# Performance work log

Measured on AMD Instinct MI355X. Metric: run time of the kernel, lower is better.

The kernel has to match this reference:

```python
import jax, jax.numpy as jnp
import numpy as np

B, T0, T1, WIDTH, N, K, H = 1, 512, 1536, 2048, 16, 4, 128
T = T0 + T1
THETA = 1000000.0
ROT = H // 2          # partial_rotary_factor = 0.5 -> rotary dim 64
EPS = 1e-6
NEG = -2.3819763e38


def _rmsnorm(x, scale):
    var = jnp.mean(jnp.square(x.astype(jnp.float32)), axis=-1, keepdims=True)
    normed = x * jnp.reciprocal(jnp.sqrt(var + EPS))
    return (normed * (1.0 + scale)).astype(x.dtype)


def _rope(x, cos, sin):
    # x: [B,T,n,H]; rotate first ROT dims (rotate-half convention), pass-through rest
    xr, xp = x[..., :ROT], x[..., ROT:]
    x1, x2 = jnp.split(xr, 2, axis=-1)
    rot = jnp.concatenate([x1 * cos - x2 * sin, x2 * cos + x1 * sin], axis=-1)
    return jnp.concatenate([rot, xp], axis=-1)


def _stream(x, tm, qg_w, k_w, v_w, qn, kn):
    x = x * tm[..., None].astype(x.dtype)
    qg = jnp.einsum('btd,ndh->btnh', x, qg_w)     # [B,t,N,2H]
    q, gate = jnp.split(qg, 2, axis=-1)
    q = _rmsnorm(q, qn)
    k = _rmsnorm(jnp.einsum('btd,kdh->btkh', x, k_w), kn)
    v = jnp.einsum('btd,kdh->btkh', x, v_w)
    return q, k, v, gate


def setup_inputs():
    key = jax.random.key(0)
    ks = jax.random.split(key, 10)
    f = jnp.float32
    sd = WIDTH ** -0.5
    so = (N * H) ** -0.5
    inp = {}
    inp['x0'] = jax.random.normal(ks[0], (B, T0, WIDTH), f)
    inp['x1'] = jax.random.normal(ks[1], (B, T1, WIDTH), f)
    inp['positions'] = jnp.broadcast_to(jnp.arange(T, dtype=jnp.int32), (B, T))
    inp['attn_mask'] = jnp.broadcast_to(jnp.tril(jnp.ones((T, T), bool)), (B, T, T))
    inp['qg_w0'] = jax.random.normal(ks[2], (N, WIDTH, 2 * H), f) * sd
    inp['k_w0'] = jax.random.normal(ks[3], (K, WIDTH, H), f) * sd
    inp['v_w0'] = jax.random.normal(ks[4], (K, WIDTH, H), f) * sd
    inp['qn0'] = jnp.zeros((H,), f)
    inp['kn0'] = jnp.zeros((H,), f)
    inp['o_w0'] = jax.random.normal(ks[5], (N, H, WIDTH), f) * so
    inp['qg_w1'] = jax.random.normal(ks[6], (N, WIDTH, 2 * H), f) * sd
    inp['k_w1'] = jax.random.normal(ks[7], (K, WIDTH, H), f) * sd
    inp['v_w1'] = jax.random.normal(ks[8], (K, WIDTH, H), f) * sd
    inp['qn1'] = jnp.zeros((H,), f)
    inp['kn1'] = jnp.zeros((H,), f)
    inp['o_w1'] = jax.random.normal(ks[9], (N, H, WIDTH), f) * so
    return inp


def reference(x0, x1, positions, attn_mask,
              qg_w0, k_w0, v_w0, qn0, kn0, o_w0,
              qg_w1, k_w1, v_w1, qn1, kn1, o_w1):
    token_mask = jnp.any(attn_mask, axis=-1)  # [B,T]
    q0, k0, v0, g0 = _stream(x0, token_mask[:, :T0], qg_w0, k_w0, v_w0, qn0, kn0)
    q1, k1, v1, g1 = _stream(x1, token_mask[:, T0:], qg_w1, k_w1, v_w1, qn1, kn1)
    q = jnp.concatenate([q0, q1], axis=1)      # [B,T,N,H]
    k = jnp.concatenate([k0, k1], axis=1)      # [B,T,K,H]
    v = jnp.concatenate([v0, v1], axis=1)
    gate = jnp.concatenate([g0, g1], axis=1)

    half = ROT // 2
    inv_freq = THETA ** (-jnp.arange(half, dtype=jnp.float32) / half)
    ang = positions.astype(jnp.float32)[:, :, None] * inv_freq   # [B,T,half]
    cos = jnp.cos(ang)[:, :, None, :]
    sin = jnp.sin(ang)[:, :, None, :]
    q = _rope(q, cos, sin)
    k = _rope(k, cos, sin)
    q = q * (H ** -0.5)

    cached_k, cached_v = k, v                  # kv_cache is None (prefill)
    rep = N // K
    k = jnp.repeat(k, rep, axis=2)             # [B,T,N,H]
    v = jnp.repeat(v, rep, axis=2)

    mask = attn_mask[:, None, :, :]            # [B,1,T,S]
    logits = jnp.einsum('btnh,bsnh->bnts', q, k, preferred_element_type=jnp.float32)
    masked = jnp.where(mask, logits, NEG)
    probs = jax.nn.softmax(masked, axis=-1).astype(q.dtype)
    probs = probs * jnp.any(mask, axis=-1, keepdims=True).astype(q.dtype)
    enc = jnp.einsum('bnts,bsnh->btnh', probs, v)
    enc = enc * jax.nn.sigmoid(gate).astype(enc.dtype)
    out0 = jnp.einsum('btnh,nhd->btd', enc[:, :T0], o_w0)
    out1 = jnp.einsum('btnh,nhd->btd', enc[:, T0:], o_w1)
    return (out0, out1, cached_k, cached_v)
```

## Files before the change

kernel.cpp:

```cpp
#include <hip/hip_runtime.h>
#include <hip/hip_bf16.h>
#include <cstdint>
#include <cstddef>

#define T0_ 512
#define TT_ 2048
#define WD_ 2048
#define NH_ 16
#define KH_ 4

typedef __attribute__((ext_vector_type(8))) short short8;
typedef __attribute__((ext_vector_type(4))) short short4v;
typedef __attribute__((ext_vector_type(4))) float f32x4;

#define AS1 __attribute__((address_space(1)))
#define AS3 __attribute__((address_space(3)))

__device__ __forceinline__ ushort f2bf(float x) {
  __hip_bfloat16 h = __float2bfloat16(x);
  ushort u; __builtin_memcpy(&u, &h, 2); return u;
}
__device__ __forceinline__ float bf2f(ushort u) {
  __hip_bfloat16 h; __builtin_memcpy(&h, &u, 2);
  return __bfloat162float(h);
}
__device__ __forceinline__ void g2l16(const ushort* g, AS3 ushort* s) {
  __builtin_amdgcn_global_load_lds((const AS1 uint32_t*)g, (AS3 uint32_t*)s, 16, 0, 0);
}

__global__ __launch_bounds__(256) void convert_x(
    const float* __restrict__ x0, const float* __restrict__ x1, ushort* __restrict__ xb)
{
  const int i = blockIdx.x * 256 + threadIdx.x;
  const int e = i * 4;
  const int row = e >> 11, col = e & 2047;
  const float* src = (row < T0_) ? (x0 + (size_t)row * WD_ + col)
                                 : (x1 + (size_t)(row - T0_) * WD_ + col);
  const float4 v = *(const float4*)src;
  ushort4 o; o.x = f2bf(v.x); o.y = f2bf(v.y); o.z = f2bf(v.z); o.w = f2bf(v.w);
  *(ushort4*)(xb + e) = o;
}

__global__ __launch_bounds__(256) void convtrans(
    const float* __restrict__ in, ushort* __restrict__ out, int R, int C)
{
  __shared__ float tile[32][33];
  const int z = blockIdx.z;
  in  += (size_t)z * R * C;
  out += (size_t)z * R * C;
  const int r0 = blockIdx.x * 32, c0 = blockIdx.y * 32;
  const int tx = threadIdx.x & 31, ty = threadIdx.x >> 5;
#pragma unroll
  for (int i = 0; i < 4; ++i)
    tile[ty + 8 * i][tx] = in[(size_t)(r0 + ty + 8 * i) * C + c0 + tx];
  __syncthreads();
#pragma unroll
  for (int i = 0; i < 4; ++i)
    out[(size_t)(c0 + ty + 8 * i) * R + r0 + tx] = f2bf(tile[tx][ty + 8 * i]);
}

__global__ __launch_bounds__(256) void convtrans2(
    const float* __restrict__ s0, const float* __restrict__ s1,
    ushort* __restrict__ d0, ushort* __restrict__ d1, int R, int C, int half)
{
  __shared__ float tile[32][33];
  int z = blockIdx.z;
  const float* in; ushort* out;
  if (z < half) { in = s0 + (size_t)z * R * C; out = d0 + (size_t)z * R * C; }
  else { z -= half; in = s1 + (size_t)z * R * C; out = d1 + (size_t)z * R * C; }
  const int r0 = blockIdx.x * 32, c0 = blockIdx.y * 32;
  const int tx = threadIdx.x & 31, ty = threadIdx.x >> 5;
#pragma unroll
  for (int i = 0; i < 4; ++i)
    tile[ty + 8 * i][tx] = in[(size_t)(r0 + ty + 8 * i) * C + c0 + tx];
  __syncthreads();
#pragma unroll
  for (int i = 0; i < 4; ++i)
    out[(size_t)(c0 + ty + 8 * i) * R + r0 + tx] = f2bf(tile[tx][ty + 8 * i]);
}

__device__ __forceinline__ void gemm_core(
    const ushort* __restrict__ A, const ushort* __restrict__ Bt,
    int row0, int col0, ushort* As, ushort* Bs, f32x4 (&acc)[4][4])
{
  const int tid = threadIdx.x;
  const int w = tid >> 6, l = tid & 63, lq = l >> 4, lm = l & 15;
  const int wr = (w >> 1) * 64, wc = (w & 1) * 64;
  const int sx = lm & 7;
  const int gsw = (tid & 7) ^ ((tid >> 3) & 7);
  const ushort* Ag = A + (size_t)(row0 + (tid >> 3)) * WD_ + gsw * 8;
  const ushort* Bg = Bt + (size_t)(col0 + (tid >> 3)) * WD_ + gsw * 8;
  AS3 ushort* AsW = (AS3 ushort*)As + w * 512;
  AS3 ushort* BsW = (AS3 ushort*)Bs + w * 512;

  auto stage = [&](int buf, int k0) {
#pragma unroll
    for (int c = 0; c < 4; ++c) {
      g2l16(Ag + (size_t)(c * 32) * WD_ + k0, AsW + buf * 8192 + c * 2048);
      g2l16(Bg + (size_t)(c * 32) * WD_ + k0, BsW + buf * 8192 + c * 2048);
    }
  };

  stage(0, 0);
  __syncthreads();
  int buf = 0;
  for (int k0 = 0; k0 < WD_; k0 += 64) {
    if (k0 + 64 < WD_) stage(buf ^ 1, k0 + 64);
    const ushort* Ab = As + buf * 8192;
    const ushort* Bb = Bs + buf * 8192;
#pragma unroll
    for (int kk = 0; kk < 2; ++kk) {
      short8 af[4], bfr[4];
#pragma unroll
      for (int mi = 0; mi < 4; ++mi)
        af[mi] = *(const short8*)&Ab[(wr + mi * 16 + lm) * 64 + (((kk * 4 + lq) ^ sx) << 3)];
#pragma unroll
      for (int ni = 0; ni < 4; ++ni)
        bfr[ni] = *(const short8*)&Bb[(wc + ni * 16 + lm) * 64 + (((kk * 4 + lq) ^ sx) << 3)];
#pragma unroll
      for (int mi = 0; mi < 4; ++mi)
#pragma unroll
        for (int ni = 0; ni < 4; ++ni)
          acc[mi][ni] = __builtin_amdgcn_mfma_f32_16x16x32_bf16(af[mi], bfr[ni], acc[mi][ni], 0, 0, 0);
    }
    __syncthreads();
    buf ^= 1;
  }
}

__global__ __launch_bounds__(256) void gemm_proj(
    const ushort* __restrict__ A,
    const ushort* __restrict__ qg0t, const ushort* __restrict__ qg1t,
    const ushort* __restrict__ k0t,  const ushort* __restrict__ k1t,
    const ushort* __restrict__ v0t,  const ushort* __restrict__ v1t,
    ushort* __restrict__ Cqg, float* __restrict__ kc, float* __restrict__ vc)
{
  __shared__ ushort As[16384], Bs[16384];
  const int bx = blockIdx.x;
  const int row0 = blockIdx.y * 128;
  const bool s1 = (row0 >= T0_);
  const ushort* Bt; int col0;
  float* Cf = nullptr; ushort* Cb = nullptr; int ldc;
  if (bx < 32) {
    Bt = s1 ? qg1t : qg0t; col0 = bx * 128; Cb = Cqg; ldc = 4096;
  } else if (bx < 36) {
    Bt = s1 ? k1t : k0t; col0 = (bx - 32) * 128; Cf = kc; ldc = 512;
  } else {
    Bt = s1 ? v1t : v0t; col0 = (bx - 36) * 128; Cf = vc; ldc = 512;
  }
  f32x4 acc[4][4];
#pragma unroll
  for (int mi = 0; mi < 4; ++mi)
#pragma unroll
    for (int ni = 0; ni < 4; ++ni) acc[mi][ni] = (f32x4){0.f, 0.f, 0.f, 0.f};
  gemm_core(A, Bt, row0, col0, As, Bs, acc);
  const int w = threadIdx.x >> 6, l = threadIdx.x & 63, lq = l >> 4, lm = l & 15;
  const int wr = (w >> 1) * 64, wc = (w & 1) * 64;
#pragma unroll
  for (int mi = 0; mi < 4; ++mi)
#pragma unroll
    for (int ni = 0; ni < 4; ++ni)
#pragma unroll
      for (int r = 0; r < 4; ++r) {
        const size_t rr = (size_t)row0 + wr + mi * 16 + lq * 4 + r;
        const size_t cc = (size_t)col0 + wc + ni * 16 + lm;
        if (Cb) Cb[rr * ldc + cc] = f2bf(acc[mi][ni][r]);
        else    Cf[rr * ldc + cc] = acc[mi][ni][r];
      }
}

__global__ __launch_bounds__(256) void gemm_out(
    const ushort* __restrict__ A, const ushort* __restrict__ W0t,
    const ushort* __restrict__ W1t, float* __restrict__ C)
{
  __shared__ ushort As[16384], Bs[16384];
  const int row0 = blockIdx.y * 128, col0 = blockIdx.x * 128;
  const ushort* Bt = (row0 < T0_) ? W0t : W1t;
  f32x4 acc[4][4];
#pragma unroll
  for (int mi = 0; mi < 4; ++mi)
#pragma unroll
    for (int ni = 0; ni < 4; ++ni) acc[mi][ni] = (f32x4){0.f, 0.f, 0.f, 0.f};
  gemm_core(A, Bt, row0, col0, As, Bs, acc);
  const int w = threadIdx.x >> 6, l = threadIdx.x & 63, lq = l >> 4, lm = l & 15;
  const int wr = (w >> 1) * 64, wc = (w & 1) * 64;
#pragma unroll
  for (int mi = 0; mi < 4; ++mi)
#pragma unroll
    for (int ni = 0; ni < 4; ++ni)
#pragma unroll
      for (int r = 0; r < 4; ++r) {
        const size_t rr = (size_t)row0 + wr + mi * 16 + lq * 4 + r;
        const size_t cc = (size_t)col0 + wc + ni * 16 + lm;
        C[rr * 2048 + cc] = acc[mi][ni][r];
      }
}

__global__ __launch_bounds__(256) void postproc(
    ushort* __restrict__ qgb, float* __restrict__ kc, ushort* __restrict__ Kb,
    const int* __restrict__ positions,
    const float* __restrict__ qn0, const float* __restrict__ kn0,
    const float* __restrict__ qn1, const float* __restrict__ kn1)
{
  const int t = blockIdx.x;
  const int w = threadIdx.x >> 6, l = threadIdx.x & 63;
  const float pos = (float)positions[t];
  const bool str1 = (t >= T0_);
  const float* qn = str1 ? qn1 : qn0;
  const float* kn = str1 ? kn1 : kn0;
  const float kfreq = 13.815510557964274f / 32.0f;
  const int h0 = 2 * l, h1 = 2 * l + 1;

  for (int r = w; r < NH_ + KH_; r += 4) {
    const bool isq = (r < NH_);
    float v0, v1; size_t bi; const float* sc;
    if (isq) {
      bi = ((size_t)t * NH_ + r) * 256;
      v0 = bf2f(qgb[bi + h0]); v1 = bf2f(qgb[bi + h1]); sc = qn;
    } else {
      bi = ((size_t)t * KH_ + (r - NH_)) * 128;
      v0 = kc[bi + h0]; v1 = kc[bi + h1]; sc = kn;
    }
    float ss = v0 * v0 + v1 * v1;
#pragma unroll
    for (int off = 32; off > 0; off >>= 1) ss += __shfl_xor(ss, off);
    const float rstd = rsqrtf(ss * (1.0f / 128.0f) + 1e-6f);
    v0 = v0 * rstd * (1.0f + sc[h0]);
    v1 = v1 * rstd * (1.0f + sc[h1]);
    const float p0 = __shfl_xor(v0, 16);
    const float p1 = __shfl_xor(v1, 16);
    if (l < 32) {
      const int i0 = (l < 16) ? h0 : (h0 - 32);
      const float a0 = pos * __expf(-(float)i0 * kfreq);
      const float a1 = pos * __expf(-(float)(i0 + 1) * kfreq);
      const float c0 = cosf(a0), s0 = sinf(a0);
      const float c1 = cosf(a1), s1v = sinf(a1);
      if (l < 16) { v0 = v0 * c0 - p0 * s0; v1 = v1 * c1 - p1 * s1v; }
      else        { v0 = v0 * c0 + p0 * s0; v1 = v1 * c1 + p1 * s1v; }
    }
    if (isq) {
      v0 *= 0.08838834764831843f; v1 *= 0.08838834764831843f;
      qgb[bi + h0] = f2bf(v0); qgb[bi + h1] = f2bf(v1);
    } else {
      kc[bi + h0] = v0; kc[bi + h1] = v1;
      Kb[bi + h0] = f2bf(v0); Kb[bi + h1] = f2bf(v1);
    }
  }
}

__global__ __launch_bounds__(256) void attn(
    const ushort* __restrict__ qgb, const ushort* __restrict__ Kb,
    const ushort* __restrict__ Vt, ushort* __restrict__ encb)
{
  __shared__ ushort Ks[2 * 16384];
  __shared__ ushort Vs[2 * 16384];
  __shared__ ushort Ps[4 * 2048];
  const int tid = threadIdx.x;
  const int w = tid >> 6, l = tid & 63, lq = l >> 4, lm = l & 15;
  const int n = blockIdx.y, kh = n >> 2;

  auto stage = [&](int buf, int s0) {
#pragma unroll
    for (int c = 0; c < 8; ++c) {
      const int row = w * 32 + c * 4 + lq;
      const int ch = lm ^ (row & 15);
      const int dst = buf * 16384 + (w * 32 + c * 4) * 128;
      g2l16(Kb + (size_t)(s0 + row) * 512 + kh * 128 + ch * 8, (AS3 ushort*)Ks + dst);
      g2l16(Vt + (size_t)(kh * 128 + row) * 2048 + s0 + ch * 8, (AS3 ushort*)Vs + dst);
    }
  };

  for (int half = 0; half < 2; ++half) {
    const int qt = half ? (31 - (int)blockIdx.x) : (int)blockIdx.x;
    const int qtb = qt * 64;
    const int nst = qt / 2 + 1;

    short8 aq[4];
    {
      const ushort* qb = qgb + ((size_t)(qtb + w * 16 + lm) * NH_ + n) * 256 + lq * 8;
#pragma unroll
      for (int kk = 0; kk < 4; ++kk) aq[kk] = *(const short8*)(qb + kk * 32);
    }
    f32x4 acc[8];
#pragma unroll
    for (int i = 0; i < 8; ++i) acc[i] = (f32x4){0.f, 0.f, 0.f, 0.f};
    float mq = -3.0e38f, lsum = 0.0f;

    __syncthreads();
    stage(0, 0);

    for (int st = 0; st < nst; ++st) {
      const int buf = st & 1;
      const int s0 = st * 128;
      __syncthreads();
      if (st + 1 < nst) stage(buf ^ 1, s0 + 128);
      const ushort* Kt = Ks + buf * 16384;
      const ushort* Vb = Vs + buf * 16384;

      f32x4 sa[8];
#pragma unroll
      for (int mi = 0; mi < 8; ++mi) sa[mi] = (f32x4){0.f, 0.f, 0.f, 0.f};
#pragma unroll
      for (int kk = 0; kk < 4; ++kk)
#pragma unroll
        for (int mi = 0; mi < 8; ++mi) {
          const short8 ak = *(const short8*)&Kt[(mi * 16 + lm) * 128 + ((kk * 4 + lq) ^ lm) * 8];
          sa[mi] = __builtin_amdgcn_mfma_f32_16x16x32_bf16(ak, aq[kk], sa[mi], 0, 0, 0);
        }
      if (s0 + 127 > qtb) {
        const int qg_ = qtb + w * 16 + lm;
#pragma unroll
        for (int mi = 0; mi < 8; ++mi)
#pragma unroll
          for (int r = 0; r < 4; ++r)
            if (s0 + mi * 16 + lq * 4 + r > qg_) sa[mi][r] = -3.0e38f;
      }
      float mx = sa[0][0];
#pragma unroll
      for (int mi = 0; mi < 8; ++mi)
#pragma unroll
        for (int r = 0; r < 4; ++r) mx = fmaxf(mx, sa[mi][r]);
      mx = fmaxf(mx, __shfl_xor(mx, 16));
      mx = fmaxf(mx, __shfl_xor(mx, 32));
      const float mn = fmaxf(mq, mx);
      const float alpha = __expf(mq - mn);
      mq = mn;
      float sl = 0.0f;
#pragma unroll
      for (int mi = 0; mi < 8; ++mi)
#pragma unroll
        for (int r = 0; r < 4; ++r) {
          const float p = __expf(sa[mi][r] - mn);
          sa[mi][r] = p; sl += p;
        }
      sl += __shfl_xor(sl, 16);
      sl += __shfl_xor(sl, 32);
      lsum = lsum * alpha + sl;

#pragma unroll
      for (int mi = 0; mi < 8; ++mi) {
        short4v pw;
#pragma unroll
        for (int r = 0; r < 4; ++r) pw[r] = (short)f2bf(sa[mi][r]);
        *(short4v*)&Ps[w * 2048 + lm * 128 + (((mi * 4 + lq)) ^ lm) * 4] = pw;
      }
      float aP[4];
#pragma unroll
      for (int r = 0; r < 4; ++r) aP[r] = __shfl(alpha, lq * 4 + r);
#pragma unroll
      for (int hi = 0; hi < 8; ++hi) {
        f32x4 a = acc[hi];
#pragma unroll
        for (int r = 0; r < 4; ++r) a[r] *= aP[r];
        acc[hi] = a;
      }
#pragma unroll
      for (int mi2 = 0; mi2 < 4; ++mi2) {
        const short4v pa = *(const short4v*)&Ps[w * 2048 + lm * 128 + ((mi2 * 8 + lq * 2 + 0) ^ lm) * 4];
        const short4v pb = *(const short4v*)&Ps[w * 2048 + lm * 128 + ((mi2 * 8 + lq * 2 + 1) ^ lm) * 4];
        const short8 ap = __builtin_shufflevector(pa, pb, 0, 1, 2, 3, 4, 5, 6, 7);
#pragma unroll
        for (int hi = 0; hi < 8; ++hi) {
          const short8 bv = *(const short8*)&Vb[(hi * 16 + lm) * 128 + ((mi2 * 4 + lq) ^ lm) * 8];
          acc[hi] = __builtin_amdgcn_mfma_f32_16x16x32_bf16(ap, bv, acc[hi], 0, 0, 0);
        }
      }
    }
    const float linv = 1.0f / lsum;
    float lP[4];
#pragma unroll
    for (int r = 0; r < 4; ++r) lP[r] = __shfl(linv, lq * 4 + r);
#pragma unroll
    for (int hi = 0; hi < 8; ++hi)
#pragma unroll
      for (int r = 0; r < 4; ++r) {
        const int t = qtb + w * 16 + lq * 4 + r;
        const int h = hi * 16 + lm;
        const float g = bf2f(qgb[((size_t)t * NH_ + n) * 256 + 128 + h]);
        const float o = acc[hi][r] * lP[r] * (1.0f / (1.0f + __expf(-g)));
        encb[((size_t)t * NH_ + n) * 128 + h] = f2bf(o);
      }
  }
}

extern "C" void kernel_launch(void* const* d_in, const int* in_sizes, int n_in,
                              void* d_out, int out_size, void* d_ws, size_t ws_size,
                              hipStream_t stream)
{
  (void)in_sizes; (void)n_in; (void)out_size; (void)ws_size;
  const float* x0    = (const float*)d_in[0];
  const float* x1    = (const float*)d_in[1];
  const int*   pos   = (const int*)d_in[2];
  const float* qg_w0 = (const float*)d_in[4];
  const float* k_w0  = (const float*)d_in[5];
  const float* v_w0  = (const float*)d_in[6];
  const float* qn0   = (const float*)d_in[7];
  const float* kn0   = (const float*)d_in[8];
  const float* o_w0  = (const float*)d_in[9];
  const float* qg_w1 = (const float*)d_in[10];
  const float* k_w1  = (const float*)d_in[11];
  const float* v_w1  = (const float*)d_in[12];
  const float* qn1   = (const float*)d_in[13];
  const float* kn1   = (const float*)d_in[14];
  const float* o_w1  = (const float*)d_in[15];

  float* out    = (float*)d_out;
  float* kcache = out + (size_t)TT_ * WD_;
  float* vcache = kcache + (size_t)TT_ * KH_ * 128;
  ushort* qsc = (ushort*)d_out;

  ushort* wbuf = (ushort*)d_ws;
  ushort* xb   = wbuf + 8388608;
  ushort* qgb  = xb + 4194304;
  ushort* encb = qgb + 8388608;
  ushort* Kbuf = xb;
  ushort* Vtb  = xb + 1048576;
  ushort* k0t = encb, *k1t = encb + 1048576, *v0t = encb + 2097152, *v1t = encb + 3145728;

  convert_x<<<4096, 256, 0, stream>>>(x0, x1, xb);

  convtrans2<<<dim3(64, 8, 32), 256, 0, stream>>>(qg_w0, qg_w1, qsc, wbuf, WD_, 256, 16);
  convtrans2<<<dim3(64, 4, 8), 256, 0, stream>>>(k_w0, k_w1, k0t, k1t, WD_, 128, 4);
  convtrans2<<<dim3(64, 4, 8), 256, 0, stream>>>(v_w0, v_w1, v0t, v1t, WD_, 128, 4);

  gemm_proj<<<dim3(40, 16), 256, 0, stream>>>(xb, qsc, wbuf, k0t, k1t, v0t, v1t,
                                              qgb, kcache, vcache);

  postproc<<<2048, 256, 0, stream>>>(qgb, kcache, Kbuf, pos, qn0, kn0, qn1, kn1);
  convtrans<<<dim3(64, 16, 1), 256, 0, stream>>>(vcache, Vtb, TT_, 512);

  attn<<<dim3(16, 16), 256, 0, stream>>>(qgb, Kbuf, Vtb, encb);

  convtrans2<<<dim3(64, 64, 2), 256, 0, stream>>>(o_w0, o_w1, wbuf, wbuf + 4194304, WD_, WD_, 1);
  gemm_out<<<dim3(16, 16), 256, 0, stream>>>(encb, wbuf, wbuf + 4194304, out);
}
```

Before: 368.9 us.

## Halve attention KV tile, give each block one query tile, fuse V transpose into postproc

The attention kernel now stages 64-key tiles instead of 128, which halves its LDS footprint. Each block handles a single query tile instead of a paired front/back tile pair, with the grid doubled to 32x16. Causal load balancing now comes from flipping the tile order for heads 8 and up. Separately, the V transpose is merged into the postproc launch as extra blocks, which removes one kernel launch. The intent is more blocks and higher occupancy in attention, at the cost of more loop iterations and syncs per key and less even per-block work.

```diff
diff --git a/kernel.cpp b/kernel.cpp
--- a/kernel.cpp
+++ b/kernel.cpp
@@ -39,24 +39,6 @@
   const float4 v = *(const float4*)src;
   ushort4 o; o.x = f2bf(v.x); o.y = f2bf(v.y); o.z = f2bf(v.z); o.w = f2bf(v.w);
   *(ushort4*)(xb + e) = o;
-}
-
-__global__ __launch_bounds__(256) void convtrans(
-    const float* __restrict__ in, ushort* __restrict__ out, int R, int C)
-{
-  __shared__ float tile[32][33];
-  const int z = blockIdx.z;
-  in  += (size_t)z * R * C;
-  out += (size_t)z * R * C;
-  const int r0 = blockIdx.x * 32, c0 = blockIdx.y * 32;
-  const int tx = threadIdx.x & 31, ty = threadIdx.x >> 5;
-#pragma unroll
-  for (int i = 0; i < 4; ++i)
-    tile[ty + 8 * i][tx] = in[(size_t)(r0 + ty + 8 * i) * C + c0 + tx];
-  __syncthreads();
-#pragma unroll
-  for (int i = 0; i < 4; ++i)
-    out[(size_t)(c0 + ty + 8 * i) * R + r0 + tx] = f2bf(tile[tx][ty + 8 * i]);
 }
 
 __global__ __launch_bounds__(256) void convtrans2(
@@ -196,12 +178,27 @@
       }
 }
 
-__global__ __launch_bounds__(256) void postproc(
+__global__ __launch_bounds__(256) void postproc_vt(
     ushort* __restrict__ qgb, float* __restrict__ kc, ushort* __restrict__ Kb,
     const int* __restrict__ positions,
     const float* __restrict__ qn0, const float* __restrict__ kn0,
-    const float* __restrict__ qn1, const float* __restrict__ kn1)
-{
+    const float* __restrict__ qn1, const float* __restrict__ kn1,
+    const float* __restrict__ vcache, ushort* __restrict__ Vtb)
+{
+  __shared__ float tile[32][33];
+  if (blockIdx.x >= 2048) {
+    const int idx = blockIdx.x - 2048;
+    const int r0 = (idx & 63) * 32, c0 = (idx >> 6) * 32;
+    const int tx = threadIdx.x & 31, ty = threadIdx.x >> 5;
+#pragma unroll
+    for (int i = 0; i < 4; ++i)
+      tile[ty + 8 * i][tx] = vcache[(size_t)(r0 + ty + 8 * i) * 512 + c0 + tx];
+    __syncthreads();
+#pragma unroll
+    for (int i = 0; i < 4; ++i)
+      Vtb[(size_t)(c0 + ty + 8 * i) * 2048 + r0 + tx] = f2bf(tile[tx][ty + 8 * i]);
+    return;
+  }
   const int t = blockIdx.x;
   const int w = threadIdx.x >> 6, l = threadIdx.x & 63;
   const float pos = (float)positions[t];
@@ -252,135 +249,140 @@
     const ushort* __restrict__ qgb, const ushort* __restrict__ Kb,
     const ushort* __restrict__ Vt, ushort* __restrict__ encb)
 {
-  __shared__ ushort Ks[2 * 16384];
-  __shared__ ushort Vs[2 * 16384];
-  __shared__ ushort Ps[4 * 2048];
+  __shared__ ushort Ks[2 * 8192];
+  __shared__ ushort Vs[2 * 8192];
+  __shared__ ushort Ps[4 * 1024];
   const int tid = threadIdx.x;
   const int w = tid >> 6, l = tid & 63, lq = l >> 4, lm = l & 15;
   const int n = blockIdx.y, kh = n >> 2;
+  const int qt = (n < 8) ? (int)blockIdx.x : (31 - (int)blockIdx.x);
+  const int qtb = qt * 64;
+  const int nst = qt + 1;
 
   auto stage = [&](int buf, int s0) {
 #pragma unroll
-    for (int c = 0; c < 8; ++c) {
-      const int row = w * 32 + c * 4 + lq;
-      const int ch = lm ^ (row & 15);
-      const int dst = buf * 16384 + (w * 32 + c * 4) * 128;
-      g2l16(Kb + (size_t)(s0 + row) * 512 + kh * 128 + ch * 8, (AS3 ushort*)Ks + dst);
-      g2l16(Vt + (size_t)(kh * 128 + row) * 2048 + s0 + ch * 8, (AS3 ushort*)Vs + dst);
+    for (int c = 0; c < 4; ++c) {
+      {
+        const int base = c * 16 + w * 4;
+        const int row = base + (l >> 4);
+        const int j = l & 15;
+        g2l16(Kb + (size_t)(s0 + row) * 512 + kh * 128 + (j ^ (row & 15)) * 8,
+              (AS3 ushort*)Ks + buf * 8192 + base * 128);
+      }
+      {
+        const int base = c * 32 + w * 8;
+        const int row = base + (l >> 3);
+        const int j = l & 7;
+        g2l16(Vt + (size_t)(kh * 128 + row) * 2048 + s0 + (j ^ (row & 7)) * 8,
+              (AS3 ushort*)Vs + buf * 8192 + base * 64);
+      }
     }
   };
 
-  for (int half = 0; half < 2; ++half) {
-    const int qt = half ? (31 - (int)blockIdx.x) : (int)blockIdx.x;
-    const int qtb = qt * 64;
-    const int nst = qt / 2 + 1;
-
-    short8 aq[4];
-    {
-      const ushort* qb = qgb + ((size_t)(qtb + w * 16 + lm) * NH_ + n) * 256 + lq * 8;
-#pragma unroll
-      for (int kk = 0; kk < 4; ++kk) aq[kk] = *(const short8*)(qb + kk * 32);
-    }
-    f32x4 acc[8];
-#pragma unroll
-    for (int i = 0; i < 8; ++i) acc[i] = (f32x4){0.f, 0.f, 0.f, 0.f};
-    float mq = -3.0e38f, lsum = 0.0f;
-
+  short8 aq[4];
+  {
+    const ushort* qb = qgb + ((size_t)(qtb + w * 16 + lm) * NH_ + n) * 256 + lq * 8;
+#pragma unroll
+    for (int kk = 0; kk < 4; ++kk) aq[kk] = *(const short8*)(qb + kk * 32);
+  }
+  f32x4 acc[8];
+#pragma unroll
+  for (int i = 0; i < 8; ++i) acc[i] = (f32x4){0.f, 0.f, 0.f, 0.f};
+  float mq = -3.0e38f, lsum = 0.0f;
+
+  stage(0, 0);
+
+  for (int st = 0; st < nst; ++st) {
+    const int buf = st & 1;
+    const int s0 = st * 64;
     __syncthreads();
-    stage(0, 0);
-
-    for (int st = 0; st < nst; ++st) {
-      const int buf = st & 1;
-      const int s0 = st * 128;
-      __syncthreads();
-      if (st + 1 < nst) stage(buf ^ 1, s0 + 128);
-      const ushort* Kt = Ks + buf * 16384;
-      const ushort* Vb = Vs + buf * 16384;
-
-      f32x4 sa[8];
-#pragma unroll
-      for (int mi = 0; mi < 8; ++mi) sa[mi] = (f32x4){0.f, 0.f, 0.f, 0.f};
-#pragma unroll
-      for (int kk = 0; kk < 4; ++kk)
-#pragma unroll
-        for (int mi = 0; mi < 8; ++mi) {
-          const short8 ak = *(const short8*)&Kt[(mi * 16 + lm) * 128 + ((kk * 4 + lq) ^ lm) * 8];
-          sa[mi] = __builtin_amdgcn_mfma_f32_16x16x32_bf16(ak, aq[kk], sa[mi], 0, 0, 0);
-        }
-      if (s0 + 127 > qtb) {
-        const int qg_ = qtb + w * 16 + lm;
-#pragma unroll
-        for (int mi = 0; mi < 8; ++mi)
-#pragma unroll
-          for (int r = 0; r < 4; ++r)
-            if (s0 + mi * 16 + lq * 4 + r > qg_) sa[mi][r] = -3.0e38f;
-      }
-      float mx = sa[0][0];
-#pragma unroll
-      for (int mi = 0; mi < 8; ++mi)
-#pragma unroll
-        for (int r = 0; r < 4; ++r) mx = fmaxf(mx, sa[mi][r]);
-      mx = fmaxf(mx, __shfl_xor(mx, 16));
-      mx = fmaxf(mx, __shfl_xor(mx, 32));
-      const float mn = fmaxf(mq, mx);
-      const float alpha = __expf(mq - mn);
-      mq = mn;
-      float sl = 0.0f;
-#pragma unroll
-      for (int mi = 0; mi < 8; ++mi)
-#pragma unroll
-        for (int r = 0; r < 4; ++r) {
-          const float p = __expf(sa[mi][r] - mn);
-          sa[mi][r] = p; sl += p;
-        }
-      sl += __shfl_xor(sl, 16);
-      sl += __shfl_xor(sl, 32);
-      lsum = lsum * alpha + sl;
-
-#pragma unroll
-      for (int mi = 0; mi < 8; ++mi) {
-        short4v pw;
-#pragma unroll
-        for (int r = 0; r < 4; ++r) pw[r] = (short)f2bf(sa[mi][r]);
-        *(short4v*)&Ps[w * 2048 + lm * 128 + (((mi * 4 + lq)) ^ lm) * 4] = pw;
-      }
-      float aP[4];
-#pragma unroll
-      for (int r = 0; r < 4; ++r) aP[r] = __shfl(alpha, lq * 4 + r);
+    if (st + 1 < nst) stage(buf ^ 1, s0 + 64);
+    const ushort* Kt = Ks + buf * 8192;
+    const ushort* Vb = Vs + buf * 8192;
+
+    f32x4 sa[4];
+#pragma unroll
+    for (int mi = 0; mi < 4; ++mi) sa[mi] = (f32x4){0.f, 0.f, 0.f, 0.f};
+#pragma unroll
+    for (int kk = 0; kk < 4; ++kk)
+#pragma unroll
+      for (int mi = 0; mi < 4; ++mi) {
+        const short8 ak = *(const short8*)&Kt[(mi * 16 + lm) * 128 + ((kk * 4 + lq) ^ lm) * 8];
+        sa[mi] = __builtin_amdgcn_mfma_f32_16x16x32_bf16(ak, aq[kk], sa[mi], 0, 0, 0);
+      }
+    if (s0 + 63 > qtb) {
+      const int qg_ = qtb + w * 16 + lm;
+#pragma unroll
+      for (int mi = 0; mi < 4; ++mi)
+#pragma unroll
+        for (int r = 0; r < 4; ++r)
+          if (s0 + mi * 16 + lq * 4 + r > qg_) sa[mi][r] = -3.0e38f;
+    }
+    float mx = sa[0][0];
+#pragma unroll
+    for (int mi = 0; mi < 4; ++mi)
+#pragma unroll
+      for (int r = 0; r < 4; ++r) mx = fmaxf(mx, sa[mi][r]);
+    mx = fmaxf(mx, __shfl_xor(mx, 16));
+    mx = fmaxf(mx, __shfl_xor(mx, 32));
+    const float mn = fmaxf(mq, mx);
+    const float alpha = __expf(mq - mn);
+    mq = mn;
+    float sl = 0.0f;
+#pragma unroll
+    for (int mi = 0; mi < 4; ++mi)
+#pragma unroll
+      for (int r = 0; r < 4; ++r) {
+        const float p = __expf(sa[mi][r] - mn);
+        sa[mi][r] = p; sl += p;
+      }
+    sl += __shfl_xor(sl, 16);
+    sl += __shfl_xor(sl, 32);
+    lsum = lsum * alpha + sl;
+
+#pragma unroll
+    for (int mi = 0; mi < 4; ++mi) {
+      short4v pw;
+#pragma unroll
+      for (int r = 0; r < 4; ++r) pw[r] = (short)f2bf(sa[mi][r]);
+      *(short4v*)&Ps[w * 1024 + lm * 64 + ((mi * 4 + lq) ^ lm) * 4] = pw;
+    }
+    float aP[4];
+#pragma unroll
+    for (int r = 0; r < 4; ++r) aP[r] = __shfl(alpha, lq * 4 + r);
+#pragma unroll
+    for (int hi = 0; hi < 8; ++hi) {
+      f32x4 a = acc[hi];
+#pragma unroll
+      for (int r = 0; r < 4; ++r) a[r] *= aP[r];
+      acc[hi] = a;
+    }
+#pragma unroll
+    for (int mi2 = 0; mi2 < 2; ++mi2) {
+      const short4v pa = *(const short4v*)&Ps[w * 1024 + lm * 64 + ((mi2 * 8 + lq * 2 + 0) ^ lm) * 4];
+      const short4v pb = *(const short4v*)&Ps[w * 1024 + lm * 64 + ((mi2 * 8 + lq * 2 + 1) ^ lm) * 4];
+      const short8 ap = __builtin_shufflevector(pa, pb, 0, 1, 2, 3, 4, 5, 6, 7);
 #pragma unroll
       for (int hi = 0; hi < 8; ++hi) {
-        f32x4 a = acc[hi];
-#pragma unroll
-        for (int r = 0; r < 4; ++r) a[r] *= aP[r];
-        acc[hi] = a;
-      }
-#pragma unroll
-      for (int mi2 = 0; mi2 < 4; ++mi2) {
-        const short4v pa = *(const short4v*)&Ps[w * 2048 + lm * 128 + ((mi2 * 8 + lq * 2 + 0) ^ lm) * 4];
-        const short4v pb = *(const short4v*)&Ps[w * 2048 + lm * 128 + ((mi2 * 8 + lq * 2 + 1) ^ lm) * 4];
-        const short8 ap = __builtin_shufflevector(pa, pb, 0, 1, 2, 3, 4, 5, 6, 7);
-#pragma unroll
-        for (int hi = 0; hi < 8; ++hi) {
-          const short8 bv = *(const short8*)&Vb[(hi * 16 + lm) * 128 + ((mi2 * 4 + lq) ^ lm) * 8];
-          acc[hi] = __builtin_amdgcn_mfma_f32_16x16x32_bf16(ap, bv, acc[hi], 0, 0, 0);
-        }
-      }
-    }
-    const float linv = 1.0f / lsum;
-    float lP[4];
-#pragma unroll
-    for (int r = 0; r < 4; ++r) lP[r] = __shfl(linv, lq * 4 + r);
-#pragma unroll
-    for (int hi = 0; hi < 8; ++hi)
-#pragma unroll
-      for (int r = 0; r < 4; ++r) {
-        const int t = qtb + w * 16 + lq * 4 + r;
-        const int h = hi * 16 + lm;
-        const float g = bf2f(qgb[((size_t)t * NH_ + n) * 256 + 128 + h]);
-        const float o = acc[hi][r] * lP[r] * (1.0f / (1.0f + __expf(-g)));
-        encb[((size_t)t * NH_ + n) * 128 + h] = f2bf(o);
-      }
-  }
+        const short8 bv = *(const short8*)&Vb[(hi * 16 + lm) * 64 + (((mi2 * 4 + lq) ^ (lm & 7)) << 3)];
+        acc[hi] = __builtin_amdgcn_mfma_f32_16x16x32_bf16(ap, bv, acc[hi], 0, 0, 0);
+      }
+    }
+  }
+  const float linv = 1.0f / lsum;
+  float lP[4];
+#pragma unroll
+  for (int r = 0; r < 4; ++r) lP[r] = __shfl(linv, lq * 4 + r);
+#pragma unroll
+  for (int hi = 0; hi < 8; ++hi)
+#pragma unroll
+    for (int r = 0; r < 4; ++r) {
+      const int t = qtb + w * 16 + lq * 4 + r;
+      const int h = hi * 16 + lm;
+      const float g = bf2f(qgb[((size_t)t * NH_ + n) * 256 + 128 + h]);
+      const float o = acc[hi][r] * lP[r] * (1.0f / (1.0f + __expf(-g)));
+      encb[((size_t)t * NH_ + n) * 128 + h] = f2bf(o);
+    }
 }
 
 extern "C" void kernel_launch(void* const* d_in, const int* in_sizes, int n_in,
@@ -426,10 +428,10 @@
   gemm_proj<<<dim3(40, 16), 256, 0, stream>>>(xb, qsc, wbuf, k0t, k1t, v0t, v1t,
                                               qgb, kcache, vcache);
 
-  postproc<<<2048, 256, 0, stream>>>(qgb, kcache, Kbuf, pos, qn0, kn0, qn1, kn1);
-  convtrans<<<dim3(64, 16, 1), 256, 0, stream>>>(vcache, Vtb, TT_, 512);
-
-  attn<<<dim3(16, 16), 256, 0, stream>>>(qgb, Kbuf, Vtb, encb);
+  postproc_vt<<<3072, 256, 0, stream>>>(qgb, kcache, Kbuf, pos, qn0, kn0, qn1, kn1,
+                                        vcache, Vtb);
+
+  attn<<<dim3(32, 16), 256, 0, stream>>>(qgb, Kbuf, Vtb, encb);
 
   convtrans2<<<dim3(64, 64, 2), 256, 0, stream>>>(o_w0, o_w1, wbuf, wbuf + 4194304, WD_, WD_, 1);
   gemm_out<<<dim3(16, 16), 256, 0, stream>>>(encb, wbuf, wbuf + 4194304, out);
```

Result: no change. 374.0 us (+1.4%).
